# Kernel tuning notes

Measured on AMD Instinct MI355X. Metric: run time of the kernel, lower is better.

The kernel has to match this reference:

```python
import jax, jax.numpy as jnp
import numpy as np
import math

HIDDEN = 4096
N_HEADS = 32
HEAD_DIM = HIDDEN // N_HEADS
ADAPTER_LEN = 10
BATCH = 1
SEQ = 2048
ROPE_BASE = 10000.0


def setup_inputs() -> dict:
    key = jax.random.key(0)
    ks = jax.random.split(key, 8)
    hidden_states = jax.random.normal(ks[0], (BATCH, SEQ, HIDDEN), dtype=jnp.float32)
    # additive causal mask [B,1,q,kv] with 0 on allowed, large negative on masked
    neg = jnp.finfo(jnp.float32).min
    causal = jnp.triu(jnp.full((SEQ, SEQ), neg, dtype=jnp.float32), k=1)
    attention_mask = jnp.broadcast_to(causal, (BATCH, 1, SEQ, SEQ))
    position_ids = jnp.broadcast_to(jnp.arange(SEQ, dtype=jnp.int64 if jax.config.read('jax_enable_x64') else jnp.int32)[None, :], (BATCH, SEQ))
    s = 0.02
    Wq = jax.random.normal(ks[1], (HIDDEN, HIDDEN), dtype=jnp.float32) * s
    Wk = jax.random.normal(ks[2], (HIDDEN, HIDDEN), dtype=jnp.float32) * s
    Wv = jax.random.normal(ks[3], (HIDDEN, HIDDEN), dtype=jnp.float32) * s
    Wo = jax.random.normal(ks[4], (HIDDEN, HIDDEN), dtype=jnp.float32) * s
    adapter_prefix = jax.random.normal(ks[5], (ADAPTER_LEN, HIDDEN), dtype=jnp.float32) * s
    gate = jnp.zeros((N_HEADS, 1, 1), dtype=jnp.float32) + 0.1  # nonzero so gated path is exercised
    return {"hidden_states": hidden_states, "attention_mask": attention_mask,
            "position_ids": position_ids, "Wq": Wq, "Wk": Wk, "Wv": Wv, "Wo": Wo,
            "adapter_prefix": adapter_prefix, "gate": gate}


def _rotate_half(x):
    x1, x2 = jnp.split(x, 2, axis=-1)
    return jnp.concatenate([-x2, x1], axis=-1)


def _rope_cos_sin(position_ids, head_dim, dtype):
    # inv_freq: [hd/2]
    inv_freq = 1.0 / (ROPE_BASE ** (jnp.arange(0, head_dim, 2, dtype=jnp.float32) / head_dim))
    freqs = position_ids.astype(jnp.float32)[:, :, None] * inv_freq[None, None, :]  # [B,S,hd/2]
    emb = jnp.concatenate([freqs, freqs], axis=-1)  # [B,S,hd]
    cos = jnp.cos(emb)[:, None, :, :].astype(dtype)  # [B,1,S,hd]
    sin = jnp.sin(emb)[:, None, :, :].astype(dtype)
    return cos, sin


def reference(hidden_states, attention_mask, position_ids, Wq, Wk, Wv, Wo, adapter_prefix, gate):
    B, S, H = hidden_states.shape
    nh, hd = N_HEADS, HEAD_DIM
    plen = adapter_prefix.shape[0]

    def proj(x, W):  # torch Linear: x @ W.T
        return jnp.einsum('...h,oh->...o', x, W)

    q = proj(hidden_states, Wq).reshape(B, S, nh, hd).transpose(0, 2, 1, 3)  # [B,nh,S,hd]
    k = proj(hidden_states, Wk).reshape(B, S, nh, hd).transpose(0, 2, 1, 3)
    v = proj(hidden_states, Wv).reshape(B, S, nh, hd).transpose(0, 2, 1, 3)

    cos, sin = _rope_cos_sin(position_ids, hd, q.dtype)
    q = q * cos + _rotate_half(q) * sin
    k = k * cos + _rotate_half(k) * sin

    # adapter prefix KV (bsz must be 1 per original view semantics; no RoPE applied)
    kp = proj(adapter_prefix, Wk).reshape(B, plen, nh, hd).transpose(0, 2, 1, 3)  # [B,nh,plen,hd]
    vp = proj(adapter_prefix, Wv).reshape(B, plen, nh, hd).transpose(0, 2, 1, 3)
    K = jnp.concatenate([kp, k], axis=2)  # [B,nh,plen+S,hd]
    V = jnp.concatenate([vp, v], axis=2)

    mask = jnp.concatenate([jnp.zeros((B, 1, S, plen), dtype=attention_mask.dtype), attention_mask], axis=-1)
    scores = jnp.einsum('bhqd,bhkd->bhqk', q, K) / math.sqrt(hd)
    scores = scores + mask
    scores = jnp.maximum(scores, jnp.finfo(scores.dtype).min)

    prefix_w = jax.nn.softmax(scores[..., :plen].astype(jnp.float32), axis=-1).astype(q.dtype)
    token_w = jax.nn.softmax(scores[..., plen:].astype(jnp.float32), axis=-1).astype(q.dtype)
    g = jnp.tanh(gate)[None, :, :, :]  # [1,nh,1,1]
    attn = jnp.concatenate([g * prefix_w, token_w], axis=-1)  # [B,nh,S,plen+S]

    out = jnp.einsum('bhqk,bhkd->bhqd', attn, V)  # [B,nh,S,hd]
    out = out.transpose(0, 2, 1, 3).reshape(B, S, H)
    return proj(out, Wo)
```

## Files before the change

### kernel.cpp

```cpp
#include <hip/hip_runtime.h>
#include <math.h>

#define HIDDEN 4096
#define NH 32
#define HD 128
#define PLEN 10
#define SEQQ 2048
#define QT 32
#define KT 64
#define QKVLD 12288

typedef __attribute__((ext_vector_type(8))) _Float16 f16x8;
typedef __attribute__((ext_vector_type(4))) float f32x4;

#define GLD16(g, l) __builtin_amdgcn_global_load_lds( \
        (const __attribute__((address_space(1))) void*)(g), \
        (__attribute__((address_space(3))) void*)(l), 16, 0, 0)

__global__ __launch_bounds__(256) void cvt_f16_kernel(
    const float* __restrict__ x, _Float16* __restrict__ y, int n8)
{
    int idx = blockIdx.x * 256 + threadIdx.x;
    if (idx >= n8) return;
    const float4* xp = (const float4*)x;
    float4 a = xp[idx * 2], b = xp[idx * 2 + 1];
    f16x8 o;
    o[0] = (_Float16)a.x; o[1] = (_Float16)a.y; o[2] = (_Float16)a.z; o[3] = (_Float16)a.w;
    o[4] = (_Float16)b.x; o[5] = (_Float16)b.y; o[6] = (_Float16)b.z; o[7] = (_Float16)b.w;
    *(f16x8*)(y + (size_t)idx * 8) = o;
}

__global__ __launch_bounds__(256) void cvt_pad_f16_kernel(
    const float* __restrict__ src, _Float16* __restrict__ y)
{
    int idx = blockIdx.x * 256 + threadIdx.x;
    int row = idx >> 9;
    f16x8 o;
    if (row < PLEN) {
        const float4* xp = (const float4*)src;
        float4 a = xp[idx * 2], b = xp[idx * 2 + 1];
        o[0] = (_Float16)a.x; o[1] = (_Float16)a.y; o[2] = (_Float16)a.z; o[3] = (_Float16)a.w;
        o[4] = (_Float16)b.x; o[5] = (_Float16)b.y; o[6] = (_Float16)b.z; o[7] = (_Float16)b.w;
    } else {
#pragma unroll
        for (int i = 0; i < 8; ++i) o[i] = (_Float16)0.0f;
    }
    *(f16x8*)(y + (size_t)idx * 8) = o;
}

template <typename OT>
__global__ __launch_bounds__(256) void gemm_f16_kernel(
    const _Float16* __restrict__ A, const _Float16* __restrict__ B,
    OT* __restrict__ C, int N, int K, int Mstore)
{
    __shared__ _Float16 lds[2 * 8192];

    const int tid = threadIdx.x;
    const int lane = tid & 63;
    const int wave = tid >> 6;

    const int gx = gridDim.x;
    const int gy = gridDim.y;
    const int nwg = gx * gy;
    const int flat = blockIdx.y * gx + blockIdx.x;
    const int cpx = nwg >> 3;
    const int sw = (flat & 7) * cpx + (flat >> 3);
    const int m0 = (sw % gy) * 128;
    const int n0 = (sw / gy) * 128;

    const _Float16* srcp = (wave < 2) ? A : B;
    const int tb = ((wave < 2) ? m0 : n0) + (wave & 1) * 64;
    const int swz = ((lane & 7) ^ ((lane >> 3) & 7)) << 3;
    const _Float16* p0 = srcp + (size_t)(tb + (lane >> 3)) * K + swz;
    _Float16* ldsw = &lds[(wave >> 1) * 8192 + (wave & 1) * 4096];

    const int lr = lane & 15;
    const int lq = lane >> 4;
    const int wm = (wave >> 1) * 64;
    const int wn = (wave & 1) * 64;

    f32x4 acc[4][4];
#pragma unroll
    for (int m = 0; m < 4; ++m)
#pragma unroll
        for (int n = 0; n < 4; ++n) acc[m][n] = (f32x4){0.f, 0.f, 0.f, 0.f};

#pragma unroll
    for (int c = 0; c < 8; ++c)
        GLD16(p0 + (size_t)c * 8 * K, ldsw + c * 512);

    const int NK = K >> 6;
    for (int ks = 0; ks < NK; ++ks) {
        __syncthreads();

#pragma unroll
        for (int kc = 0; kc < 2; ++kc) {
            f16x8 af[4], bf[4];
#pragma unroll
            for (int m = 0; m < 4; ++m) {
                int r = wm + m * 16 + lr;
                af[m] = *(const f16x8*)&lds[(r << 6) + ((((kc << 2) + lq) ^ (lr & 7)) << 3)];
            }
#pragma unroll
            for (int n = 0; n < 4; ++n) {
                int r = wn + n * 16 + lr;
                bf[n] = *(const f16x8*)&lds[8192 + (r << 6) + ((((kc << 2) + lq) ^ (lr & 7)) << 3)];
            }
            __builtin_amdgcn_s_setprio(1);
#pragma unroll
            for (int m = 0; m < 4; ++m)
#pragma unroll
                for (int n = 0; n < 4; ++n)
                    acc[m][n] = __builtin_amdgcn_mfma_f32_16x16x32_f16(af[m], bf[n], acc[m][n], 0, 0, 0);
            __builtin_amdgcn_s_setprio(0);
        }

        __syncthreads();
        if (ks + 1 < NK) {
            const int k0 = (ks + 1) << 6;
#pragma unroll
            for (int c = 0; c < 8; ++c)
                GLD16(p0 + (size_t)c * 8 * K + k0, ldsw + c * 512);
        }
    }

#pragma unroll
    for (int m = 0; m < 4; ++m) {
        const int row = m0 + wm + m * 16 + lq * 4;
#pragma unroll
        for (int n = 0; n < 4; ++n) {
            const int col = n0 + wn + n * 16 + lr;
#pragma unroll
            for (int j = 0; j < 4; ++j)
                if (row + j < Mstore)
                    C[(size_t)(row + j) * N + col] = (OT)acc[m][n][j];
        }
    }
}

__global__ void rope_table_kernel(const int* __restrict__ pos,
                                  float* __restrict__ cosT, float* __restrict__ sinT)
{
    int s = blockIdx.x;
    int j = threadIdx.x;
    float p = (float)pos[s];
    float expnt = (2.0f * (float)j) * (1.0f / 128.0f);
    float inv_freq = powf(10000.0f, -expnt);
    float f = p * inv_freq;
    cosT[s * 64 + j] = cosf(f);
    sinT[s * 64 + j] = sinf(f);
}

__global__ void rope_f16ip_kernel(_Float16* __restrict__ qkv,
                                  const float* __restrict__ cosT, const float* __restrict__ sinT)
{
    int idx = blockIdx.x * 256 + threadIdx.x;
    int s = idx >> 11;
    int rem = idx & 2047;
    int h = rem >> 6;
    int d = rem & 63;
    float c = cosT[s * 64 + d], sn = sinT[s * 64 + d];
    size_t base = (size_t)s * QKVLD + h * HD + d;
    float a = (float)qkv[base], b = (float)qkv[base + 64];
    qkv[base]      = (_Float16)(a * c - b * sn);
    qkv[base + 64] = (_Float16)(b * c + a * sn);
    size_t kb = base + HIDDEN;
    a = (float)qkv[kb]; b = (float)qkv[kb + 64];
    qkv[kb]      = (_Float16)(a * c - b * sn);
    qkv[kb + 64] = (_Float16)(b * c + a * sn);
}

__global__ __launch_bounds__(256) void vtrans_f16_kernel(
    const _Float16* __restrict__ v, _Float16* __restrict__ vt)
{
    __shared__ _Float16 Vsh[64][136];
    const int h = blockIdx.y;
    const int s0 = blockIdx.x * 64;
    const int tid = threadIdx.x;
#pragma unroll
    for (int i = 0; i < 4; ++i) {
        int flat = tid + 256 * i;
        int r = flat >> 4;
        int c8 = (flat & 15) * 8;
        *(f16x8*)&Vsh[r][c8] = *(const f16x8*)(v + (size_t)(s0 + r) * QKVLD + h * HD + c8);
    }
    __syncthreads();
#pragma unroll
    for (int pass = 0; pass < 4; ++pass) {
        int d = pass * 32 + (tid >> 3);
        int sb = (tid & 7) * 8;
        f16x8 o;
#pragma unroll
        for (int e = 0; e < 8; ++e) o[e] = Vsh[sb + e][d];
        *(f16x8*)(vt + ((size_t)h * HD + d) * SEQQ + s0 + sb) = o;
    }
}

__global__ __launch_bounds__(256) void attn_f16_kernel(
    const _Float16* __restrict__ Qf, const _Float16* __restrict__ Kf,
    const _Float16* __restrict__ Vtf,
    const float* __restrict__ kp, const float* __restrict__ vp,
    const float* __restrict__ gate, _Float16* __restrict__ out)
{
    __shared__ _Float16 Ks[64 * 128];
    __shared__ _Float16 Vs[128 * 64];
    __shared__ _Float16 Psh[4][16][72];
    __shared__ float Pp[4][16][12];

    const int h = blockIdx.x;
    const int qt = (gridDim.y - 1) - blockIdx.y;
    const int q0 = qt * 64;
    const int tid = threadIdx.x;
    const int wave = tid >> 6;
    const int lane = tid & 63;
    const int lr = lane & 15;
    const int lq = lane >> 4;
    const float scale = 0.088388347648318447f;
    const float scale2 = 0.088388347648318447f * 1.4426950408889634f;

    const int qrow = q0 + wave * 16 + lr;
    f16x8 qh[4];
#pragma unroll
    for (int c = 0; c < 4; ++c)
        qh[c] = *(const f16x8*)(Qf + (size_t)qrow * QKVLD + h * HD + c * 32 + lq * 8);

    f32x4 accO[8];
#pragma unroll
    for (int n = 0; n < 8; ++n) accO[n] = (f32x4){0.f, 0.f, 0.f, 0.f};
    float m_run[4] = {-INFINITY, -INFINITY, -INFINITY, -INFINITY};
    float l_run[4] = {0.f, 0.f, 0.f, 0.f};

    const int ntiles = qt + 1;
    for (int t = 0; t < ntiles; ++t) {
        const int j0 = t * 64;
        __syncthreads();

        {
            const int rl = lane >> 4;
            const int ch = lane & 15;
#pragma unroll
            for (int ii = 0; ii < 4; ++ii) {
                int r = wave * 16 + ii * 4 + rl;
                int chs = ch ^ (r & 7);
                const _Float16* g = Kf + (size_t)(j0 + r) * QKVLD + h * HD + chs * 8;
                GLD16(g, &Ks[(wave * 16 + ii * 4) * 128]);
            }
        }
        {
            const int dl = lane >> 3;
            const int vch = lane & 7;
#pragma unroll
            for (int ii = 0; ii < 4; ++ii) {
                int d = wave * 32 + ii * 8 + dl;
                int chs = vch ^ (d & 7);
                const _Float16* g = Vtf + ((size_t)h * HD + d) * SEQQ + j0 + chs * 8;
                GLD16(g, &Vs[(wave * 32 + ii * 8) * 64]);
            }
        }
        __syncthreads();

        f32x4 sacc[4];
#pragma unroll
        for (int n = 0; n < 4; ++n) sacc[n] = (f32x4){0.f, 0.f, 0.f, 0.f};
        __builtin_amdgcn_s_setprio(1);
#pragma unroll
        for (int c = 0; c < 4; ++c) {
#pragma unroll
            for (int n = 0; n < 4; ++n) {
                int row = n * 16 + lr;
                int chs = (4 * c + lq) ^ (lr & 7);
                f16x8 kf8 = *(const f16x8*)&Ks[row * 128 + chs * 8];
                sacc[n] = __builtin_amdgcn_mfma_f32_16x16x32_f16(qh[c], kf8, sacc[n], 0, 0, 0);
            }
        }
        __builtin_amdgcn_s_setprio(0);

#pragma unroll
        for (int j = 0; j < 4; ++j) {
            const int grow = q0 + wave * 16 + lq * 4 + j;
#pragma unroll
            for (int n = 0; n < 4; ++n) {
                int gcol = j0 + n * 16 + lr;
                float val = sacc[n][j] * scale2;
                sacc[n][j] = (gcol > grow) ? -INFINITY : val;
            }
            float mx = fmaxf(fmaxf(sacc[0][j], sacc[1][j]), fmaxf(sacc[2][j], sacc[3][j]));
            mx = fmaxf(mx, __shfl_xor(mx, 1));
            mx = fmaxf(mx, __shfl_xor(mx, 2));
            mx = fmaxf(mx, __shfl_xor(mx, 4));
            mx = fmaxf(mx, __shfl_xor(mx, 8));
            float mn = fmaxf(m_run[j], mx);
            float corr = exp2f(m_run[j] - mn);
            m_run[j] = mn;
            float ls = 0.f;
#pragma unroll
            for (int n = 0; n < 4; ++n) {
                float p = exp2f(sacc[n][j] - mn);
                Psh[wave][lq * 4 + j][n * 16 + lr] = (_Float16)p;
                ls += p;
            }
            ls += __shfl_xor(ls, 1);
            ls += __shfl_xor(ls, 2);
            ls += __shfl_xor(ls, 4);
            ls += __shfl_xor(ls, 8);
            l_run[j] = l_run[j] * corr + ls;
#pragma unroll
            for (int n = 0; n < 8; ++n) accO[n][j] *= corr;
        }

        asm volatile("s_waitcnt lgkmcnt(0)" ::: "memory");

        __builtin_amdgcn_s_setprio(1);
#pragma unroll
        for (int jc = 0; jc < 2; ++jc) {
            f16x8 pa = *(const f16x8*)&Psh[wave][lr][jc * 32 + lq * 8];
#pragma unroll
            for (int n = 0; n < 8; ++n) {
                int row = n * 16 + lr;
                int chv = (jc * 4 + lq) ^ (lr & 7);
                f16x8 vf = *(const f16x8*)&Vs[row * 64 + chv * 8];
                accO[n] = __builtin_amdgcn_mfma_f32_16x16x32_f16(pa, vf, accO[n], 0, 0, 0);
            }
        }
        __builtin_amdgcn_s_setprio(0);
    }

#pragma unroll
    for (int j = 0; j < 4; ++j) {
        float inv_l = 1.0f / l_run[j];
#pragma unroll
        for (int n = 0; n < 8; ++n) accO[n][j] *= inv_l;
    }

    {
        float g = tanhf(gate[h]);
        float sp[PLEN];
        float mp = -INFINITY;
#pragma unroll
        for (int i = 0; i < PLEN; ++i) {
            const float* kpr = kp + (size_t)i * QKVLD + h * HD;
            float s = 0.f;
#pragma unroll
            for (int c = 0; c < 4; ++c)
#pragma unroll
                for (int e = 0; e < 8; ++e)
                    s = fmaf((float)qh[c][e], kpr[c * 32 + lq * 8 + e], s);
            s += __shfl_xor(s, 16);
            s += __shfl_xor(s, 32);
            sp[i] = s * scale;
            mp = fmaxf(mp, sp[i]);
        }
        float ssum = 0.f;
#pragma unroll
        for (int i = 0; i < PLEN; ++i) { sp[i] = expf(sp[i] - mp); ssum += sp[i]; }
        float gs = g / ssum;
        if (lq == 0) {
#pragma unroll
            for (int i = 0; i < PLEN; ++i) Pp[wave][lr][i] = sp[i] * gs;
        }
        asm volatile("s_waitcnt lgkmcnt(0)" ::: "memory");
#pragma unroll
        for (int i = 0; i < PLEN; ++i) {
            float vv[8];
#pragma unroll
            for (int n = 0; n < 8; ++n)
                vv[n] = vp[(size_t)i * QKVLD + h * HD + n * 16 + lr];
#pragma unroll
            for (int j = 0; j < 4; ++j) {
                float w = Pp[wave][lq * 4 + j][i];
#pragma unroll
                for (int n = 0; n < 8; ++n) accO[n][j] = fmaf(w, vv[n], accO[n][j]);
            }
        }
    }

#pragma unroll
    for (int n = 0; n < 8; ++n)
#pragma unroll
        for (int j = 0; j < 4; ++j)
            out[(size_t)(q0 + wave * 16 + lq * 4 + j) * HIDDEN + h * HD + n * 16 + lr] =
                (_Float16)accO[n][j];
}

__global__ __launch_bounds__(256) void gemm_nt_kernel(
    const float* __restrict__ A, const float* __restrict__ B, float* __restrict__ C,
    int M, int N, int K)
{
    __shared__ float As[8][132];
    __shared__ float Bs[8][132];
    const int tid = threadIdx.x;
    const int tx = tid & 15, ty = tid >> 4;
    const int m0 = blockIdx.y * 128, n0 = blockIdx.x * 128;
    const int lr = tid >> 1;
    const int lk = (tid & 1) * 4;
    const bool aval = (m0 + lr) < M;
    const float* Ap = A + (size_t)(m0 + lr) * K + lk;
    const float* Bp = B + (size_t)(n0 + lr) * K + lk;

    float acc[8][8];
#pragma unroll
    for (int i = 0; i < 8; ++i)
#pragma unroll
        for (int j = 0; j < 8; ++j) acc[i][j] = 0.0f;

    for (int k0 = 0; k0 < K; k0 += 8) {
        float4 a4 = make_float4(0.f, 0.f, 0.f, 0.f);
        if (aval) a4 = *(const float4*)(Ap + k0);
        float4 b4 = *(const float4*)(Bp + k0);
        __syncthreads();
        As[lk + 0][lr] = a4.x; As[lk + 1][lr] = a4.y; As[lk + 2][lr] = a4.z; As[lk + 3][lr] = a4.w;
        Bs[lk + 0][lr] = b4.x; Bs[lk + 1][lr] = b4.y; Bs[lk + 2][lr] = b4.z; Bs[lk + 3][lr] = b4.w;
        __syncthreads();
#pragma unroll
        for (int kk = 0; kk < 8; ++kk) {
            float4 a0 = *(const float4*)&As[kk][ty * 8];
            float4 a1 = *(const float4*)&As[kk][ty * 8 + 4];
            float4 b0 = *(const float4*)&Bs[kk][tx * 8];
            float4 b1 = *(const float4*)&Bs[kk][tx * 8 + 4];
            float a[8] = {a0.x, a0.y, a0.z, a0.w, a1.x, a1.y, a1.z, a1.w};
            float b[8] = {b0.x, b0.y, b0.z, b0.w, b1.x, b1.y, b1.z, b1.w};
#pragma unroll
            for (int i = 0; i < 8; ++i)
#pragma unroll
                for (int j = 0; j < 8; ++j)
                    acc[i][j] = fmaf(a[i], b[j], acc[i][j]);
        }
    }
#pragma unroll
    for (int i = 0; i < 8; ++i) {
        int row = m0 + ty * 8 + i;
        if (row < M) {
            float* Cp = C + (size_t)row * N + n0 + tx * 8;
            *(float4*)Cp       = make_float4(acc[i][0], acc[i][1], acc[i][2], acc[i][3]);
            *(float4*)(Cp + 4) = make_float4(acc[i][4], acc[i][5], acc[i][6], acc[i][7]);
        }
    }
}

__global__ void rope_apply_kernel(float* __restrict__ q, float* __restrict__ k,
                                  const float* __restrict__ cosT, const float* __restrict__ sinT)
{
    int idx = blockIdx.x * 256 + threadIdx.x;
    int s = idx >> 11;
    int rem = idx & 2047;
    int h = rem >> 6;
    int d = rem & 63;
    float c = cosT[s * 64 + d], sn = sinT[s * 64 + d];
    size_t base = (size_t)s * HIDDEN + h * HD + d;
    float a = q[base], b = q[base + 64];
    q[base]      = a * c - b * sn;
    q[base + 64] = b * c + a * sn;
    a = k[base]; b = k[base + 64];
    k[base]      = a * c - b * sn;
    k[base + 64] = b * c + a * sn;
}

__global__ __launch_bounds__(256) void attn_kernel(
    const float* __restrict__ q, const float* __restrict__ k, const float* __restrict__ v,
    const float* __restrict__ kp, const float* __restrict__ vp,
    const float* __restrict__ gate, float* __restrict__ out)
{
    __shared__ float Qt[128][36];
    __shared__ float KV[128 * 68];
    __shared__ float Psh2[QT][68];

    const int h = blockIdx.y;
    const int r0 = blockIdx.x * QT;
    const int tid = threadIdx.x;
    const int orow = tid >> 3;
    const int oc4 = (tid & 7) * 4;
    const int sy = tid >> 4;
    const int sx = tid & 15;
    const float scale = 0.088388347648318447f;

#pragma unroll
    for (int i = 0; i < 4; ++i) {
        int flat = tid + 256 * i;
        int r = flat >> 5;
        int d = (flat & 31) << 2;
        float4 t = *(const float4*)(q + (size_t)(r0 + r) * HIDDEN + h * HD + d);
        Qt[d + 0][r] = t.x; Qt[d + 1][r] = t.y; Qt[d + 2][r] = t.z; Qt[d + 3][r] = t.w;
    }

    float acc[4][4];
#pragma unroll
    for (int u = 0; u < 4; ++u)
#pragma unroll
        for (int i = 0; i < 4; ++i) acc[u][i] = 0.0f;
    float m_run = -INFINITY, l_run = 0.0f;

    const int jb_max = (r0 + QT - 1) >> 6;
    for (int jb = 0; jb <= jb_max; ++jb) {
        const int j0 = jb * KT;
        __syncthreads();
#pragma unroll
        for (int i = 0; i < 8; ++i) {
            int flat = tid + 256 * i;
            int r = flat >> 5;
            int d = (flat & 31) << 2;
            float4 t = *(const float4*)(k + (size_t)(j0 + r) * HIDDEN + h * HD + d);
            KV[(d + 0) * 68 + r] = t.x; KV[(d + 1) * 68 + r] = t.y;
            KV[(d + 2) * 68 + r] = t.z; KV[(d + 3) * 68 + r] = t.w;
        }
        __syncthreads();
        float s8[2][4] = {{0.f, 0.f, 0.f, 0.f}, {0.f, 0.f, 0.f, 0.f}};
        for (int d = 0; d < 128; ++d) {
            float2 qv = *(const float2*)&Qt[d][sy * 2];
            float4 kv4 = *(const float4*)&KV[d * 68 + sx * 4];
            s8[0][0] = fmaf(qv.x, kv4.x, s8[0][0]);
            s8[0][1] = fmaf(qv.x, kv4.y, s8[0][1]);
            s8[0][2] = fmaf(qv.x, kv4.z, s8[0][2]);
            s8[0][3] = fmaf(qv.x, kv4.w, s8[0][3]);
            s8[1][0] = fmaf(qv.y, kv4.x, s8[1][0]);
            s8[1][1] = fmaf(qv.y, kv4.y, s8[1][1]);
            s8[1][2] = fmaf(qv.y, kv4.z, s8[1][2]);
            s8[1][3] = fmaf(qv.y, kv4.w, s8[1][3]);
        }
#pragma unroll
        for (int i = 0; i < 2; ++i) {
            int gr = r0 + sy * 2 + i;
#pragma unroll
            for (int jj = 0; jj < 4; ++jj) {
                int gj = j0 + sx * 4 + jj;
                float val = s8[i][jj] * scale;
                Psh2[sy * 2 + i][sx * 4 + jj] = (gj > gr) ? -INFINITY : val;
            }
        }
        __syncthreads();
        {
            const int c0 = (tid & 7) * 8;
            float sv[8];
            float mx = -INFINITY;
#pragma unroll
            for (int i = 0; i < 8; ++i) { sv[i] = Psh2[orow][c0 + i]; mx = fmaxf(mx, sv[i]); }
            mx = fmaxf(mx, __shfl_xor(mx, 1));
            mx = fmaxf(mx, __shfl_xor(mx, 2));
            mx = fmaxf(mx, __shfl_xor(mx, 4));
            float m_new = fmaxf(m_run, mx);
            float corr = expf(m_run - m_new);
            float lsum = 0.f;
#pragma unroll
            for (int i = 0; i < 8; ++i) {
                float p = expf(sv[i] - m_new);
                Psh2[orow][c0 + i] = p;
                lsum += p;
            }
            lsum += __shfl_xor(lsum, 1);
            lsum += __shfl_xor(lsum, 2);
            lsum += __shfl_xor(lsum, 4);
            l_run = l_run * corr + lsum;
            m_run = m_new;
#pragma unroll
            for (int u = 0; u < 4; ++u)
#pragma unroll
                for (int i = 0; i < 4; ++i) acc[u][i] *= corr;
        }
        __syncthreads();
#pragma unroll
        for (int i = 0; i < 8; ++i) {
            int flat = tid + 256 * i;
            int r = flat >> 5;
            int d = (flat & 31) << 2;
            float4 t = *(const float4*)(v + (size_t)(j0 + r) * HIDDEN + h * HD + d);
            *(float4*)&KV[r * 136 + d] = t;
        }
        __syncthreads();
        for (int j = 0; j < KT; ++j) {
            float p = Psh2[orow][j];
#pragma unroll
            for (int u = 0; u < 4; ++u) {
                float4 vv = *(const float4*)&KV[j * 136 + oc4 + u * 32];
                acc[u][0] = fmaf(p, vv.x, acc[u][0]);
                acc[u][1] = fmaf(p, vv.y, acc[u][1]);
                acc[u][2] = fmaf(p, vv.z, acc[u][2]);
                acc[u][3] = fmaf(p, vv.w, acc[u][3]);
            }
        }
    }

    float inv_l = 1.0f / l_run;
#pragma unroll
    for (int u = 0; u < 4; ++u)
#pragma unroll
        for (int i = 0; i < 4; ++i) acc[u][i] *= inv_l;

    {
        float g = tanhf(gate[h]);
        float sp[PLEN];
        float mp = -INFINITY;
#pragma unroll
        for (int i = 0; i < PLEN; ++i) {
            const float* kpr = kp + (size_t)i * HIDDEN + h * HD;
            float s = 0.f;
            for (int d = 0; d < 128; ++d) s = fmaf(Qt[d][orow], kpr[d], s);
            sp[i] = s * scale;
            mp = fmaxf(mp, sp[i]);
        }
        float ssum = 0.f;
#pragma unroll
        for (int i = 0; i < PLEN; ++i) { sp[i] = expf(sp[i] - mp); ssum += sp[i]; }
        float gs = g / ssum;
#pragma unroll
        for (int i = 0; i < PLEN; ++i) {
            float w = sp[i] * gs;
            const float* vpr = vp + (size_t)i * HIDDEN + h * HD;
#pragma unroll
            for (int u = 0; u < 4; ++u) {
                float4 vv = *(const float4*)(vpr + oc4 + u * 32);
                acc[u][0] = fmaf(w, vv.x, acc[u][0]);
                acc[u][1] = fmaf(w, vv.y, acc[u][1]);
                acc[u][2] = fmaf(w, vv.z, acc[u][2]);
                acc[u][3] = fmaf(w, vv.w, acc[u][3]);
            }
        }
    }

    float* op = out + (size_t)(r0 + orow) * HIDDEN + h * HD;
#pragma unroll
    for (int u = 0; u < 4; ++u)
        *(float4*)(op + oc4 + u * 32) = make_float4(acc[u][0], acc[u][1], acc[u][2], acc[u][3]);
}

extern "C" void kernel_launch(void* const* d_in, const int* in_sizes, int n_in,
                              void* d_out, int out_size, void* d_ws, size_t ws_size,
                              hipStream_t stream)
{
    (void)in_sizes; (void)n_in; (void)out_size;
    const float* hidden  = (const float*)d_in[0];
    const int*   pos     = (const int*)d_in[2];
    const float* Wq      = (const float*)d_in[3];
    const float* Wk      = (const float*)d_in[4];
    const float* Wv      = (const float*)d_in[5];
    const float* Wo      = (const float*)d_in[6];
    const float* adapter = (const float*)d_in[7];
    const float* gate    = (const float*)d_in[8];
    float* out = (float*)d_out;

    const size_t SH = (size_t)SEQQ * HIDDEN;
    const size_t WN = (size_t)HIDDEN * HIDDEN;
    const size_t PN = (size_t)128 * HIDDEN;

    float* cosT = (float*)d_ws;
    float* sinT = cosT + (size_t)SEQQ * 64;
    float* AP   = sinT + (size_t)SEQQ * 64;
    _Float16* Hf    = (_Float16*)(AP + (size_t)128 * QKVLD);
    _Float16* Wqkvf = Hf + SH;
    _Float16* Pf    = Wqkvf + 3 * WN;
    _Float16* QKVf  = Pf + PN;
    _Float16* Vtf   = QKVf + 3 * SH;
    const size_t need = (size_t)((char*)(Vtf + SH) - (char*)d_ws);
    const bool use_f16 = (ws_size >= need);

    _Float16* Of  = Hf;
    _Float16* Wof = Wqkvf;

    rope_table_kernel<<<SEQQ, 64, 0, stream>>>(pos, cosT, sinT);

    dim3 blk(256);
    const int nH8 = (int)(SH / 8);
    const int nW8 = (int)(WN / 8);

    if (use_f16) {
        cvt_f16_kernel<<<nH8 / 256, blk, 0, stream>>>(hidden, Hf, nH8);
        cvt_f16_kernel<<<nW8 / 256, blk, 0, stream>>>(Wq, Wqkvf, nW8);
        cvt_f16_kernel<<<nW8 / 256, blk, 0, stream>>>(Wk, Wqkvf + WN, nW8);
        cvt_f16_kernel<<<nW8 / 256, blk, 0, stream>>>(Wv, Wqkvf + 2 * WN, nW8);
        cvt_pad_f16_kernel<<<(int)(PN / 8 / 256), blk, 0, stream>>>(adapter, Pf);

        gemm_f16_kernel<_Float16><<<dim3(QKVLD / 128, SEQQ / 128), blk, 0, stream>>>(
            Hf, Wqkvf, QKVf, QKVLD, HIDDEN, SEQQ);
        gemm_f16_kernel<float><<<dim3(QKVLD / 128, 1), blk, 0, stream>>>(
            Pf, Wqkvf, AP, QKVLD, HIDDEN, PLEN);

        rope_f16ip_kernel<<<(SEQQ * 2048) / 256, blk, 0, stream>>>(QKVf, cosT, sinT);
        vtrans_f16_kernel<<<dim3(SEQQ / 64, NH), blk, 0, stream>>>(QKVf + 2 * HIDDEN, Vtf);

        attn_f16_kernel<<<dim3(NH, SEQQ / 64), blk, 0, stream>>>(
            QKVf, QKVf + HIDDEN, Vtf, AP + HIDDEN, AP + 2 * HIDDEN, gate, Of);

        cvt_f16_kernel<<<nW8 / 256, blk, 0, stream>>>(Wo, Wof, nW8);
        gemm_f16_kernel<float><<<dim3(HIDDEN / 128, SEQQ / 128), blk, 0, stream>>>(
            Of, Wof, out, HIDDEN, HIDDEN, SEQQ);
    } else {
        float* ws = (float*)d_ws;
        float* qb   = ws;
        float* kb   = ws + SH;
        float* vb   = ws + 2 * SH;
        float* kpb  = ws + 3 * SH;
        float* vpb  = kpb + (size_t)PLEN * HIDDEN;
        float* cT   = vpb + (size_t)PLEN * HIDDEN;
        float* sT   = cT + (size_t)SEQQ * 64;
        rope_table_kernel<<<SEQQ, 64, 0, stream>>>(pos, cT, sT);
        dim3 gbig(HIDDEN / 128, SEQQ / 128);
        dim3 gsm(HIDDEN / 128, 1);
        gemm_nt_kernel<<<gbig, blk, 0, stream>>>(hidden, Wq, qb, SEQQ, HIDDEN, HIDDEN);
        gemm_nt_kernel<<<gbig, blk, 0, stream>>>(hidden, Wk, kb, SEQQ, HIDDEN, HIDDEN);
        gemm_nt_kernel<<<gbig, blk, 0, stream>>>(hidden, Wv, vb, SEQQ, HIDDEN, HIDDEN);
        gemm_nt_kernel<<<gsm, blk, 0, stream>>>(adapter, Wk, kpb, PLEN, HIDDEN, HIDDEN);
        gemm_nt_kernel<<<gsm, blk, 0, stream>>>(adapter, Wv, vpb, PLEN, HIDDEN, HIDDEN);
        rope_apply_kernel<<<(SEQQ * 2048) / 256, 256, 0, stream>>>(qb, kb, cT, sT);
        attn_kernel<<<dim3(SEQQ / QT, NH), blk, 0, stream>>>(qb, kb, vb, kpb, vpb, gate, qb);
        gemm_nt_kernel<<<gbig, blk, 0, stream>>>(qb, Wo, out, SEQQ, HIDDEN, HIDDEN);
    }
}
```

Baseline: 573.3 us.

## Double-buffer LDS in f16 GEMM to overlap global loads with MFMA compute

The GEMM kernel now holds two 32 KB LDS buffers and prefetches tile t+2 while tile t is being computed. Partial vmcnt waits let one stage of global-to-LDS loads stay in flight. The aim is to hide global load latency that the old single-buffer load-then-compute loop exposed. In exchange LDS use doubles to 64 KB per block, which may cut occupancy, and the hand-written waitcnt and barrier logic is fragile.

```diff
diff --git a/kernel.cpp b/kernel.cpp
--- a/kernel.cpp
+++ b/kernel.cpp
@@ -53,7 +53,7 @@
     const _Float16* __restrict__ A, const _Float16* __restrict__ B,
     OT* __restrict__ C, int N, int K, int Mstore)
 {
-    __shared__ _Float16 lds[2 * 8192];
+    __shared__ _Float16 lds[2 * 16384];
 
     const int tid = threadIdx.x;
     const int lane = tid & 63;
@@ -72,7 +72,7 @@
     const int tb = ((wave < 2) ? m0 : n0) + (wave & 1) * 64;
     const int swz = ((lane & 7) ^ ((lane >> 3) & 7)) << 3;
     const _Float16* p0 = srcp + (size_t)(tb + (lane >> 3)) * K + swz;
-    _Float16* ldsw = &lds[(wave >> 1) * 8192 + (wave & 1) * 4096];
+    const int ldso = (wave >> 1) * 8192 + (wave & 1) * 4096;
 
     const int lr = lane & 15;
     const int lq = lane >> 4;
@@ -85,26 +85,43 @@
 #pragma unroll
         for (int n = 0; n < 4; ++n) acc[m][n] = (f32x4){0.f, 0.f, 0.f, 0.f};
 
-#pragma unroll
-    for (int c = 0; c < 8; ++c)
-        GLD16(p0 + (size_t)c * 8 * K, ldsw + c * 512);
+#define STAGE(bufsel, tt) do { \
+        _Float16* dst_ = &lds[(bufsel) * 16384 + ldso]; \
+        const _Float16* src_ = p0 + ((size_t)(tt) << 6); \
+        GLD16(src_ + 0 * 8 * (size_t)K, dst_ + 0 * 512); \
+        GLD16(src_ + 1 * 8 * (size_t)K, dst_ + 1 * 512); \
+        GLD16(src_ + 2 * 8 * (size_t)K, dst_ + 2 * 512); \
+        GLD16(src_ + 3 * 8 * (size_t)K, dst_ + 3 * 512); \
+        GLD16(src_ + 4 * 8 * (size_t)K, dst_ + 4 * 512); \
+        GLD16(src_ + 5 * 8 * (size_t)K, dst_ + 5 * 512); \
+        GLD16(src_ + 6 * 8 * (size_t)K, dst_ + 6 * 512); \
+        GLD16(src_ + 7 * 8 * (size_t)K, dst_ + 7 * 512); \
+    } while (0)
 
     const int NK = K >> 6;
-    for (int ks = 0; ks < NK; ++ks) {
-        __syncthreads();
-
+    STAGE(0, 0);
+    STAGE(1, 1);
+
+    for (int t = 0; t < NK; ++t) {
+        const int cur = t & 1;
+        if (t == NK - 1) asm volatile("s_waitcnt vmcnt(0)" ::: "memory");
+        else             asm volatile("s_waitcnt vmcnt(8)" ::: "memory");
+        __builtin_amdgcn_s_barrier();
+
+        const _Float16* la = &lds[cur * 16384];
+        const _Float16* lb = &lds[cur * 16384 + 8192];
 #pragma unroll
         for (int kc = 0; kc < 2; ++kc) {
             f16x8 af[4], bf[4];
 #pragma unroll
             for (int m = 0; m < 4; ++m) {
                 int r = wm + m * 16 + lr;
-                af[m] = *(const f16x8*)&lds[(r << 6) + ((((kc << 2) + lq) ^ (lr & 7)) << 3)];
+                af[m] = *(const f16x8*)&la[(r << 6) + ((((kc << 2) + lq) ^ (lr & 7)) << 3)];
             }
 #pragma unroll
             for (int n = 0; n < 4; ++n) {
                 int r = wn + n * 16 + lr;
-                bf[n] = *(const f16x8*)&lds[8192 + (r << 6) + ((((kc << 2) + lq) ^ (lr & 7)) << 3)];
+                bf[n] = *(const f16x8*)&lb[(r << 6) + ((((kc << 2) + lq) ^ (lr & 7)) << 3)];
             }
             __builtin_amdgcn_s_setprio(1);
 #pragma unroll
@@ -114,15 +131,10 @@
                     acc[m][n] = __builtin_amdgcn_mfma_f32_16x16x32_f16(af[m], bf[n], acc[m][n], 0, 0, 0);
             __builtin_amdgcn_s_setprio(0);
         }
-
-        __syncthreads();
-        if (ks + 1 < NK) {
-            const int k0 = (ks + 1) << 6;
-#pragma unroll
-            for (int c = 0; c < 8; ++c)
-                GLD16(p0 + (size_t)c * 8 * K + k0, ldsw + c * 512);
-        }
-    }
+        __builtin_amdgcn_s_barrier();
+        if (t + 2 < NK) STAGE(cur, t + 2);
+    }
+#undef STAGE
 
 #pragma unroll
     for (int m = 0; m < 4; ++m) {
```

New measurement: 553.8 us. 1.04x faster.
